# Kernel optimization log

Hardware: AMD Instinct MI355X
Metric: run time of the kernel (lower is better)

Reference implementation:

```python
import jax, jax.numpy as jnp
from jax import lax
import numpy as np

B0 = 2          # batch
S = 32          # spatial grid side; L = S*S + 2
L = S * S + 2
DM = 256        # d_model
ED = 512        # d_inner = expand_factor * d_model
N = 16          # d_state
R = 16          # dt_rank = ceil(d_model/16)
K = 4           # d_conv


def _dwconv(x, w, b):
    # x: (B, L, ED) -> causal depthwise conv1d, kernel K, left-pad K-1 (== torch pad K-1 then [:, :, :L])
    xt = jnp.transpose(x, (0, 2, 1))  # (B, ED, L)
    o = lax.conv_general_dilated(xt, w, (1,), [(K - 1, 0)],
                                 feature_group_count=ED,
                                 dimension_numbers=('NCH', 'OIH', 'NCH'))
    return jnp.transpose(o + b[None, :, None], (0, 2, 1))


def _ssm(x, Alog, Dp, xp_w, dt_w, dt_b):
    # x: (B, L, ED); selective scan (mamba.py math, pscan=True path)
    A = -jnp.exp(Alog)                       # (ED, N)
    dBC = x @ xp_w.T                          # (B, L, R+2N)
    delta = jax.nn.softplus(dBC[..., :R] @ dt_w.T + dt_b)  # (B, L, ED)
    Bm = dBC[..., R:R + N]                    # (B, L, N)
    Cm = dBC[..., R + N:]                     # (B, L, N)
    dA = jnp.exp(delta[..., None] * A)        # (B, L, ED, N)
    dBx = (delta * x)[..., None] * Bm[:, :, None, :]  # (B, L, ED, N)

    def comb(e1, e2):
        a1, b1 = e1
        a2, b2 = e2
        return a1 * a2, a2 * b1 + b2

    _, hs = lax.associative_scan(comb, (dA, dBx), axis=1)  # h_t = dA_t*h_{t-1} + dBx_t
    return jnp.einsum('blen,bln->ble', hs, Cm) + Dp * x


def _cross(t):
    # keep first/last token, transpose the SxS interior grid (row-major <-> col-major)
    b, l, d = t.shape
    inner = t[:, 1:-1].reshape(b, S, S, d).transpose(0, 2, 1, 3).reshape(b, S * S, d)
    return jnp.concatenate([t[:, :1], inner, t[:, -1:]], axis=1)


def _branch(xz, cw, cb, xp, dw, db, Al, Dp):
    xa, za = jnp.split(xz, 2, axis=-1)
    xa = jax.nn.silu(_dwconv(xa, cw, cb))
    return _ssm(xa, Al, Dp, xp, dw, db) * jax.nn.silu(za)


def _forward(x, in_w, out_w, *p):
    xz = x @ in_w.T  # (B, L, 2*ED)
    (cwa, cba, xpa, dwa, dba, Ala, Da,
     cwb, cbb, xpb, dwb, dbb, Alb, Db,
     cwc, cbc, xpc, dwc, dbc, Alc, Dc,
     cwd, cbd, xpd, dwd, dbd, Ald, Dd) = p
    ga = _branch(xz, cwa, cba, xpa, dwa, dba, Ala, Da)                # forward scan
    gb = _branch(xz[:, ::-1], cwb, cbb, xpb, dwb, dbb, Alb, Db)       # reversed scan
    xzc = _cross(xz)
    gc = _branch(xzc, cwc, cbc, xpc, dwc, dbc, Alc, Dc)               # transposed scan
    gd = _branch(xzc[:, ::-1], cwd, cbd, xpd, dwd, dbd, Ald, Dd)      # reversed-transposed scan
    # gating commutes with token permutations, so reassemble gated outputs
    y = (ga + gb[:, ::-1] + _cross(gc) + _cross(gd)[:, ::-1]) * 0.25  # divide_output=True
    return y @ out_w.T


def setup_inputs() -> dict:
    keys = jax.random.split(jax.random.key(0), 64)
    it = iter(keys)

    def nrm(shape, scale=0.02):
        return scale * jax.random.normal(next(it), shape, dtype=jnp.float32)

    d = {}
    d['x'] = jax.random.normal(next(it), (B0, L, DM), dtype=jnp.float32)
    d['in_w'] = nrm((2 * ED, DM))
    d['out_w'] = nrm((DM, ED))
    std = R ** -0.5
    for s in ['a', 'b', 'c', 'd']:
        d[f'conv_w_{s}'] = nrm((ED, 1, K), 0.1)
        d[f'conv_b_{s}'] = jnp.zeros((ED,), jnp.float32)
        d[f'xp_w_{s}'] = nrm((R + 2 * N, ED))
        d[f'dt_w_{s}'] = jax.random.uniform(next(it), (ED, R), minval=-std, maxval=std, dtype=jnp.float32)
        dt = jnp.exp(jax.random.uniform(next(it), (ED,), dtype=jnp.float32)
                     * (np.float32(np.log(0.1)) - np.float32(np.log(0.001))) + np.float32(np.log(0.001)))
        d[f'dt_b_{s}'] = dt + jnp.log(-jnp.expm1(-dt))  # inverse-softplus init
        d[f'Alog_{s}'] = jnp.log(jnp.tile(jnp.arange(1, N + 1, dtype=jnp.float32), (ED, 1)))
        d[f'D_{s}'] = jnp.ones((ED,), jnp.float32)
    return d


def reference(x, in_w, out_w,
              conv_w_a, conv_b_a, xp_w_a, dt_w_a, dt_b_a, Alog_a, D_a,
              conv_w_b, conv_b_b, xp_w_b, dt_w_b, dt_b_b, Alog_b, D_b,
              conv_w_c, conv_b_c, xp_w_c, dt_w_c, dt_b_c, Alog_c, D_c,
              conv_w_d, conv_b_d, xp_w_d, dt_w_d, dt_b_d, Alog_d, D_d):
    return _forward(x, in_w, out_w,
                    conv_w_a, conv_b_a, xp_w_a, dt_w_a, dt_b_a, Alog_a, D_a,
                    conv_w_b, conv_b_b, xp_w_b, dt_w_b, dt_b_b, Alog_b, D_b,
                    conv_w_c, conv_b_c, xp_w_c, dt_w_c, dt_b_c, Alog_c, D_c,
                    conv_w_d, conv_b_d, xp_w_d, dt_w_d, dt_b_d, Alog_d, D_d)
```

## Files before the change

### kernel.cpp

```cpp
#include <hip/hip_runtime.h>
#include <math.h>

#define LL 1026
#define EDim 512
#define MM 2052
#define NC 8
#define LC 128

struct Params {
  const float* cw[4];
  const float* cb[4];
  const float* xpw[4];
  const float* dtw[4];
  const float* dtb[4];
  const float* Al[4];
  const float* Dp[4];
};

__device__ __forceinline__ int sigma_map(int branch, int l) {
  if (branch & 1) l = LL - 1 - l;
  if (branch & 2) {
    if (l > 0 && l < LL - 1) {
      int p = l - 1;
      l = 1 + ((p & 31) << 5) + (p >> 5);
    }
  }
  return l;
}

__device__ __forceinline__ float silu_f(float v) { return v / (1.f + expf(-v)); }

template<int CTRL>
__device__ __forceinline__ float dpp_mov0(float x) {
  int r = __builtin_amdgcn_update_dpp(0, __float_as_int(x), CTRL, 0xF, 0xF, false);
  return __int_as_float(r);
}

__global__ __launch_bounds__(256) void k1_gemm_in(
    const float* __restrict__ x, const float* __restrict__ w,
    float* __restrict__ xa, float* __restrict__ sz) {
  __shared__ float As[32][65];
  __shared__ float Bs[32][65];
  const int t = threadIdx.x;
  const int tx = t & 15, ty = t >> 4;
  const int m0 = blockIdx.x * 64, n0 = blockIdx.y * 64;
  float acc[4][4] = {};
  for (int k0 = 0; k0 < 256; k0 += 32) {
    #pragma unroll
    for (int p = 0; p < 2; ++p) {
      int f = t + p * 256;
      int row = f >> 3, cf = f & 7;
      int gr = m0 + row; gr = gr < MM ? gr : MM - 1;
      float4 v = *(const float4*)(x + (size_t)gr * 256 + k0 + cf * 4);
      As[cf*4+0][row] = v.x; As[cf*4+1][row] = v.y;
      As[cf*4+2][row] = v.z; As[cf*4+3][row] = v.w;
      int gn = n0 + row;
      float4 u = *(const float4*)(w + (size_t)gn * 256 + k0 + cf * 4);
      Bs[cf*4+0][row] = u.x; Bs[cf*4+1][row] = u.y;
      Bs[cf*4+2][row] = u.z; Bs[cf*4+3][row] = u.w;
    }
    __syncthreads();
    #pragma unroll
    for (int k = 0; k < 32; ++k) {
      float a0 = As[k][ty*4+0], a1 = As[k][ty*4+1], a2 = As[k][ty*4+2], a3 = As[k][ty*4+3];
      float b0 = Bs[k][tx*4+0], b1 = Bs[k][tx*4+1], b2 = Bs[k][tx*4+2], b3 = Bs[k][tx*4+3];
      acc[0][0]=fmaf(a0,b0,acc[0][0]); acc[0][1]=fmaf(a0,b1,acc[0][1]); acc[0][2]=fmaf(a0,b2,acc[0][2]); acc[0][3]=fmaf(a0,b3,acc[0][3]);
      acc[1][0]=fmaf(a1,b0,acc[1][0]); acc[1][1]=fmaf(a1,b1,acc[1][1]); acc[1][2]=fmaf(a1,b2,acc[1][2]); acc[1][3]=fmaf(a1,b3,acc[1][3]);
      acc[2][0]=fmaf(a2,b0,acc[2][0]); acc[2][1]=fmaf(a2,b1,acc[2][1]); acc[2][2]=fmaf(a2,b2,acc[2][2]); acc[2][3]=fmaf(a2,b3,acc[2][3]);
      acc[3][0]=fmaf(a3,b0,acc[3][0]); acc[3][1]=fmaf(a3,b1,acc[3][1]); acc[3][2]=fmaf(a3,b2,acc[3][2]); acc[3][3]=fmaf(a3,b3,acc[3][3]);
    }
    __syncthreads();
  }
  #pragma unroll
  for (int i = 0; i < 4; ++i) {
    int gm = m0 + ty*4 + i;
    if (gm < MM) {
      #pragma unroll
      for (int j = 0; j < 4; ++j) {
        int gn = n0 + tx*4 + j;
        float v = acc[i][j];
        if (gn < 512) xa[(size_t)gm*512 + gn] = v;
        else          sz[(size_t)gm*512 + gn - 512] = silu_f(v);
      }
    }
  }
}

__global__ __launch_bounds__(256) void k2_branch(
    Params P, const float* __restrict__ xa,
    float* __restrict__ xac, float* __restrict__ delta, float* __restrict__ bcg) {
  __shared__ float xcS[16][516];
  __shared__ float dBCs[16][49];
  const int t = threadIdx.x;
  const int l0 = blockIdx.x * 16;
  const int b  = blockIdx.y;
  const int br = blockIdx.z;
  const int e0 = 2 * t;
  const float* cw = P.cw[br];
  const float w00 = cw[e0*4+0], w01 = cw[e0*4+1], w02 = cw[e0*4+2], w03 = cw[e0*4+3];
  const float w10 = cw[(e0+1)*4+0], w11 = cw[(e0+1)*4+1], w12 = cw[(e0+1)*4+2], w13 = cw[(e0+1)*4+3];
  const float cb0 = P.cb[br][e0], cb1 = P.cb[br][e0+1];
  const float* xab = xa + (size_t)b * LL * 512;
  const size_t obase = (size_t)(br*2 + b) * LL;

  float h0x=0,h0y=0,h1x=0,h1y=0,h2x=0,h2y=0,h3x=0,h3y=0;
  for (int i = -3; i < 16; ++i) {
    int l = l0 + i;
    float cx = 0.f, cy = 0.f;
    if (l >= 0 && l < LL) {
      int pos = sigma_map(br, l);
      float2 v = *(const float2*)(xab + (size_t)pos * 512 + e0);
      cx = v.x; cy = v.y;
    }
    h0x=h1x; h0y=h1y; h1x=h2x; h1y=h2y; h2x=h3x; h2y=h3y; h3x=cx; h3y=cy;
    if (i >= 0) {
      float o0 = fmaf(w00,h0x, fmaf(w01,h1x, fmaf(w02,h2x, fmaf(w03,h3x, cb0))));
      float o1 = fmaf(w10,h0y, fmaf(w11,h1y, fmaf(w12,h2y, fmaf(w13,h3y, cb1))));
      o0 = silu_f(o0); o1 = silu_f(o1);
      *(float2*)&xcS[i][e0] = make_float2(o0, o1);
      if (l < LL)
        *(float2*)(xac + (obase + l) * 512 + e0) = make_float2(o0, o1);
    }
  }
  __syncthreads();

  const int rowi = t & 15;
  const int r0 = t >> 4;
  const float* xpw = P.xpw[br];
  const float4* xr4 = (const float4*)&xcS[rowi][0];
  const float4* wa = (const float4*)(xpw + (size_t)r0 * 512);
  const float4* wb = (const float4*)(xpw + (size_t)(r0 + 16) * 512);
  const float4* wc = (const float4*)(xpw + (size_t)(r0 + 32) * 512);
  float acc0 = 0.f, acc1 = 0.f, acc2 = 0.f;
  #pragma unroll 8
  for (int e4 = 0; e4 < 128; ++e4) {
    float4 xv = xr4[e4];
    float4 a = wa[e4], bb = wb[e4], c = wc[e4];
    acc0 = fmaf(xv.x,a.x, fmaf(xv.y,a.y, fmaf(xv.z,a.z, fmaf(xv.w,a.w, acc0))));
    acc1 = fmaf(xv.x,bb.x,fmaf(xv.y,bb.y,fmaf(xv.z,bb.z,fmaf(xv.w,bb.w,acc1))));
    acc2 = fmaf(xv.x,c.x, fmaf(xv.y,c.y, fmaf(xv.z,c.z, fmaf(xv.w,c.w, acc2))));
  }
  dBCs[rowi][r0]      = acc0;
  dBCs[rowi][r0 + 16] = acc1;
  dBCs[rowi][r0 + 32] = acc2;
  __syncthreads();

  for (int idx = t; idx < 512; idx += 256) {
    int row = idx >> 5, c = idx & 31;
    int l = l0 + row;
    if (l < LL) bcg[(obase + l)*32 + c] = dBCs[row][16 + c];
  }

  const float* dtw = P.dtw[br];
  float dw0[16], dw1[16];
  #pragma unroll
  for (int r = 0; r < 16; ++r) { dw0[r] = dtw[e0*16 + r]; dw1[r] = dtw[(e0+1)*16 + r]; }
  const float db0 = P.dtb[br][e0], db1 = P.dtb[br][e0+1];
  for (int row = 0; row < 16; ++row) {
    int l = l0 + row;
    if (l >= LL) break;
    float s0 = db0, s1 = db1;
    #pragma unroll
    for (int r = 0; r < 16; ++r) {
      float d = dBCs[row][r];
      s0 = fmaf(d, dw0[r], s0);
      s1 = fmaf(d, dw1[r], s1);
    }
    float sp0 = fmaxf(s0, 0.f) + log1pf(expf(-fabsf(s0)));
    float sp1 = fmaxf(s1, 0.f) + log1pf(expf(-fabsf(s1)));
    *(float2*)(delta + (obase + l)*512 + e0) = make_float2(sp0, sp1);
  }
}

__global__ __launch_bounds__(256) void k3a_chunk(
    Params P, const float* __restrict__ xac, const float* __restrict__ delta,
    const float* __restrict__ bcg, float* __restrict__ Pc, float* __restrict__ Qc) {
  __shared__ float dT[16][33], xT[16][33], bT[16][33];
  const int t = threadIdx.x;
  const int eL = t >> 4, n = t & 15;
  const int e0 = blockIdx.x * 16;
  const int b = blockIdx.y;
  const int br = blockIdx.z / NC, c = blockIdx.z % NC;
  const size_t sbase = (size_t)(br*2 + b) * LL;
  const float* dl = delta + sbase * 512;
  const float* xc = xac + sbase * 512;
  const float* bc = bcg + sbase * 32;
  const float A_en = -expf(P.Al[br][(e0 + eL)*16 + n]);
  const int l0 = c * LC;
  const int lend = (c == NC-1) ? LL : (l0 + LC);
  float h = 0.f, dsum = 0.f;

  for (int c0 = l0; c0 < lend; c0 += 32) {
    #pragma unroll
    for (int p = 0; p < 2; ++p) {
      int idx = t + p*256;
      int s = idx >> 4, ee = idx & 15;
      int l = c0 + s;
      float dv = 0.f, xv = 0.f, bv = 0.f;
      if (l < lend) {
        dv = dl[(size_t)l*512 + e0 + ee];
        xv = xc[(size_t)l*512 + e0 + ee];
        bv = bc[l*32 + ee];
      }
      dT[ee][s] = dv; xT[ee][s] = xv; bT[ee][s] = bv;
    }
    __syncthreads();
    float da[32], dbx[32];
    #pragma unroll
    for (int s = 0; s < 32; ++s) {
      float d = dT[eL][s];
      da[s]  = __expf(d * A_en);
      dbx[s] = d * xT[eL][s] * bT[n][s];
      dsum += d;
    }
    #pragma unroll
    for (int s = 0; s < 32; ++s) h = fmaf(da[s], h, dbx[s]);
    __syncthreads();
  }
  size_t oi = ((((size_t)(br*2 + b)*NC + c)*32 + blockIdx.x)*256 + t);
  Pc[oi] = __expf(dsum * A_en);
  Qc[oi] = h;
}

__global__ __launch_bounds__(256) void k3b_scan(
    Params P, const float* __restrict__ xac, const float* __restrict__ delta,
    const float* __restrict__ bcg, const float* __restrict__ sz,
    const float* __restrict__ Pc, const float* __restrict__ Qc,
    float* __restrict__ g) {
  __shared__ float dT[16][33], xT[16][33], bT[16][33], cT[16][33];
  __shared__ float ybuf[32][17];
  const int t = threadIdx.x;
  const int eL = t >> 4, n = t & 15;
  const int e0 = blockIdx.x * 16;
  const int b = blockIdx.y;
  const int br = blockIdx.z / NC, c = blockIdx.z % NC;
  const size_t sbase = (size_t)(br*2 + b) * LL;
  const float* dl = delta + sbase * 512;
  const float* xc = xac + sbase * 512;
  const float* bc = bcg + sbase * 32;
  const float A_en = -expf(P.Al[br][(e0 + eL)*16 + n]);
  const float Dval = P.Dp[br][e0 + (t & 15)];
  const float* szb = sz + (size_t)b * LL * 512;
  float* gb = g + (size_t)br * MM * 512 + (size_t)b * LL * 512;

  float h = 0.f;
  for (int cc = 0; cc < c; ++cc) {
    size_t ii = ((((size_t)(br*2 + b)*NC + cc)*32 + blockIdx.x)*256 + t);
    h = fmaf(Pc[ii], h, Qc[ii]);
  }

  const int l0c = c * LC;
  const int lend = (c == NC-1) ? LL : (l0c + LC);
  for (int c0 = l0c; c0 < lend; c0 += 32) {
    #pragma unroll
    for (int p = 0; p < 2; ++p) {
      int idx = t + p*256;
      int s = idx >> 4, ee = idx & 15;
      int l = c0 + s;
      float dv = 0.f, xv = 0.f, bv = 0.f, cv = 0.f;
      if (l < lend) {
        dv = dl[(size_t)l*512 + e0 + ee];
        xv = xc[(size_t)l*512 + e0 + ee];
        bv = bc[l*32 + ee];
        cv = bc[l*32 + 16 + ee];
      }
      dT[ee][s] = dv; xT[ee][s] = xv; bT[ee][s] = bv; cT[ee][s] = cv;
    }
    __syncthreads();

    float da[32], dbx[32], ccv[32];
    #pragma unroll
    for (int s = 0; s < 32; ++s) {
      float d  = dT[eL][s];
      float xv = xT[eL][s];
      da[s]  = __expf(d * A_en);
      dbx[s] = d * xv * bT[n][s];
      ccv[s] = cT[n][s];
    }
    #pragma unroll
    for (int s = 0; s < 32; ++s) {
      h = fmaf(da[s], h, dbx[s]);
      float r = h * ccv[s];
      r += dpp_mov0<0xB1>(r);
      r += dpp_mov0<0x4E>(r);
      r += dpp_mov0<0x114>(r);
      r += dpp_mov0<0x118>(r);
      if (n == 15) ybuf[s][eL] = r;
    }
    __syncthreads();

    #pragma unroll
    for (int p = 0; p < 2; ++p) {
      int idx = t + p*256;
      int s = idx >> 4, ee = idx & 15;
      int l = c0 + s;
      if (l < lend) {
        float yv = fmaf(Dval, xT[ee][s], ybuf[s][ee]);
        int pos = sigma_map(br, l);
        float szv = szb[(size_t)pos * 512 + e0 + ee];
        gb[(size_t)pos * 512 + e0 + ee] = yv * szv;
      }
    }
    __syncthreads();
  }
}

__global__ __launch_bounds__(256) void k4_gemm_out(
    const float* __restrict__ g, const float* __restrict__ w, float* __restrict__ out) {
  __shared__ float As[32][65];
  __shared__ float Bs[32][33];
  const int t = threadIdx.x;
  const int tx = t & 15, ty = t >> 4;
  const int m0 = blockIdx.x * 64, n0 = blockIdx.y * 32;
  const float* g1 = g + (size_t)MM*512;
  const float* g2 = g + (size_t)2*MM*512;
  const float* g3 = g + (size_t)3*MM*512;
  float acc[4][2] = {};
  for (int k0 = 0; k0 < 512; k0 += 32) {
    #pragma unroll
    for (int p = 0; p < 8; ++p) {
      int idx = t + p*256;
      int row = idx >> 5, kk = idx & 31;
      int gm = m0 + row; gm = gm < MM ? gm : MM - 1;
      size_t ga = (size_t)gm*512 + k0 + kk;
      As[kk][row] = 0.25f * (g[ga] + g1[ga] + g2[ga] + g3[ga]);
    }
    #pragma unroll
    for (int p = 0; p < 4; ++p) {
      int idx = t + p*256;
      int row = idx >> 5, kk = idx & 31;
      Bs[kk][row] = w[(size_t)(n0 + row)*512 + k0 + kk];
    }
    __syncthreads();
    #pragma unroll
    for (int k = 0; k < 32; ++k) {
      float a0 = As[k][ty*4+0], a1 = As[k][ty*4+1], a2 = As[k][ty*4+2], a3 = As[k][ty*4+3];
      float b0 = Bs[k][tx*2+0], b1 = Bs[k][tx*2+1];
      acc[0][0]=fmaf(a0,b0,acc[0][0]); acc[0][1]=fmaf(a0,b1,acc[0][1]);
      acc[1][0]=fmaf(a1,b0,acc[1][0]); acc[1][1]=fmaf(a1,b1,acc[1][1]);
      acc[2][0]=fmaf(a2,b0,acc[2][0]); acc[2][1]=fmaf(a2,b1,acc[2][1]);
      acc[3][0]=fmaf(a3,b0,acc[3][0]); acc[3][1]=fmaf(a3,b1,acc[3][1]);
    }
    __syncthreads();
  }
  #pragma unroll
  for (int i = 0; i < 4; ++i) {
    int gm = m0 + ty*4 + i;
    if (gm < MM) {
      out[(size_t)gm*256 + n0 + tx*2 + 0] = acc[i][0];
      out[(size_t)gm*256 + n0 + tx*2 + 1] = acc[i][1];
    }
  }
}

extern "C" void kernel_launch(void* const* d_in, const int* in_sizes, int n_in,
                              void* d_out, int out_size, void* d_ws, size_t ws_size,
                              hipStream_t stream) {
  const float* x    = (const float*)d_in[0];
  const float* in_w = (const float*)d_in[1];
  const float* out_w= (const float*)d_in[2];
  Params prm;
  for (int s = 0; s < 4; ++s) {
    prm.cw[s]  = (const float*)d_in[3 + s*7 + 0];
    prm.cb[s]  = (const float*)d_in[3 + s*7 + 1];
    prm.xpw[s] = (const float*)d_in[3 + s*7 + 2];
    prm.dtw[s] = (const float*)d_in[3 + s*7 + 3];
    prm.dtb[s] = (const float*)d_in[3 + s*7 + 4];
    prm.Al[s]  = (const float*)d_in[3 + s*7 + 5];
    prm.Dp[s]  = (const float*)d_in[3 + s*7 + 6];
  }
  float* ws = (float*)d_ws;
  const size_t SZ1 = (size_t)MM * 512;
  float* xa   = ws;
  float* szp  = ws + SZ1;
  float* xac  = ws + 2*SZ1;
  float* dlt  = ws + 6*SZ1;
  float* bc   = ws + 10*SZ1;
  float* gbuf = ws + 10*SZ1 + (size_t)4*MM*32;
  float* Pc = xa;
  float* Qc = xa + (size_t)8*NC*32*256;

  k1_gemm_in<<<dim3(33, 16), 256, 0, stream>>>(x, in_w, xa, szp);
  k2_branch <<<dim3(65, 2, 4), 256, 0, stream>>>(prm, xa, xac, dlt, bc);
  k3a_chunk <<<dim3(32, 2, 4*NC), 256, 0, stream>>>(prm, xac, dlt, bc, Pc, Qc);
  k3b_scan  <<<dim3(32, 2, 4*NC), 256, 0, stream>>>(prm, xac, dlt, bc, szp, Pc, Qc, gbuf);
  k4_gemm_out<<<dim3(33, 8), 256, 0, stream>>>(gbuf, out_w, (float*)d_out);
}
```

Before: 330.5 us.

## Shrink k2 and k4 tiles for more blocks; vectorize shared loads in GEMMs

```diff
diff --git a/kernel.cpp b/kernel.cpp
--- a/kernel.cpp
+++ b/kernel.cpp
@@ -39,8 +39,8 @@
 __global__ __launch_bounds__(256) void k1_gemm_in(
     const float* __restrict__ x, const float* __restrict__ w,
     float* __restrict__ xa, float* __restrict__ sz) {
-  __shared__ float As[32][65];
-  __shared__ float Bs[32][65];
+  __shared__ float As[32][68];
+  __shared__ float Bs[32][68];
   const int t = threadIdx.x;
   const int tx = t & 15, ty = t >> 4;
   const int m0 = blockIdx.x * 64, n0 = blockIdx.y * 64;
@@ -62,8 +62,10 @@
     __syncthreads();
     #pragma unroll
     for (int k = 0; k < 32; ++k) {
-      float a0 = As[k][ty*4+0], a1 = As[k][ty*4+1], a2 = As[k][ty*4+2], a3 = As[k][ty*4+3];
-      float b0 = Bs[k][tx*4+0], b1 = Bs[k][tx*4+1], b2 = Bs[k][tx*4+2], b3 = Bs[k][tx*4+3];
+      float4 av = *(const float4*)&As[k][ty*4];
+      float4 bv = *(const float4*)&Bs[k][tx*4];
+      float a0 = av.x, a1 = av.y, a2 = av.z, a3 = av.w;
+      float b0 = bv.x, b1 = bv.y, b2 = bv.z, b3 = bv.w;
       acc[0][0]=fmaf(a0,b0,acc[0][0]); acc[0][1]=fmaf(a0,b1,acc[0][1]); acc[0][2]=fmaf(a0,b2,acc[0][2]); acc[0][3]=fmaf(a0,b3,acc[0][3]);
       acc[1][0]=fmaf(a1,b0,acc[1][0]); acc[1][1]=fmaf(a1,b1,acc[1][1]); acc[1][2]=fmaf(a1,b2,acc[1][2]); acc[1][3]=fmaf(a1,b3,acc[1][3]);
       acc[2][0]=fmaf(a2,b0,acc[2][0]); acc[2][1]=fmaf(a2,b1,acc[2][1]); acc[2][2]=fmaf(a2,b2,acc[2][2]); acc[2][3]=fmaf(a2,b3,acc[2][3]);
@@ -89,10 +91,10 @@
 __global__ __launch_bounds__(256) void k2_branch(
     Params P, const float* __restrict__ xa,
     float* __restrict__ xac, float* __restrict__ delta, float* __restrict__ bcg) {
-  __shared__ float xcS[16][516];
-  __shared__ float dBCs[16][49];
-  const int t = threadIdx.x;
-  const int l0 = blockIdx.x * 16;
+  __shared__ float xcS[8][516];
+  __shared__ float dBCs[8][2][52];
+  const int t = threadIdx.x;
+  const int l0 = blockIdx.x * 8;
   const int b  = blockIdx.y;
   const int br = blockIdx.z;
   const int e0 = 2 * t;
@@ -104,7 +106,7 @@
   const size_t obase = (size_t)(br*2 + b) * LL;
 
   float h0x=0,h0y=0,h1x=0,h1y=0,h2x=0,h2y=0,h3x=0,h3y=0;
-  for (int i = -3; i < 16; ++i) {
+  for (int i = -3; i < 8; ++i) {
     int l = l0 + i;
     float cx = 0.f, cy = 0.f;
     if (l >= 0 && l < LL) {
@@ -124,31 +126,33 @@
   }
   __syncthreads();
 
-  const int rowi = t & 15;
-  const int r0 = t >> 4;
+  const int combo = t & 15;
+  const int prow = combo >> 1, phalf = combo & 1;
+  const int tg = t >> 4;
   const float* xpw = P.xpw[br];
-  const float4* xr4 = (const float4*)&xcS[rowi][0];
-  const float4* wa = (const float4*)(xpw + (size_t)r0 * 512);
-  const float4* wb = (const float4*)(xpw + (size_t)(r0 + 16) * 512);
-  const float4* wc = (const float4*)(xpw + (size_t)(r0 + 32) * 512);
+  const float4* xr4 = (const float4*)&xcS[prow][phalf*256];
+  const float4* wa = (const float4*)(xpw + (size_t)tg*512        + phalf*256);
+  const float4* wb = (const float4*)(xpw + (size_t)(tg+16)*512   + phalf*256);
+  const float4* wc = (const float4*)(xpw + (size_t)(tg+32)*512   + phalf*256);
   float acc0 = 0.f, acc1 = 0.f, acc2 = 0.f;
   #pragma unroll 8
-  for (int e4 = 0; e4 < 128; ++e4) {
+  for (int e4 = 0; e4 < 64; ++e4) {
     float4 xv = xr4[e4];
     float4 a = wa[e4], bb = wb[e4], c = wc[e4];
     acc0 = fmaf(xv.x,a.x, fmaf(xv.y,a.y, fmaf(xv.z,a.z, fmaf(xv.w,a.w, acc0))));
     acc1 = fmaf(xv.x,bb.x,fmaf(xv.y,bb.y,fmaf(xv.z,bb.z,fmaf(xv.w,bb.w,acc1))));
     acc2 = fmaf(xv.x,c.x, fmaf(xv.y,c.y, fmaf(xv.z,c.z, fmaf(xv.w,c.w, acc2))));
   }
-  dBCs[rowi][r0]      = acc0;
-  dBCs[rowi][r0 + 16] = acc1;
-  dBCs[rowi][r0 + 32] = acc2;
+  dBCs[prow][phalf][tg]      = acc0;
+  dBCs[prow][phalf][tg + 16] = acc1;
+  dBCs[prow][phalf][tg + 32] = acc2;
   __syncthreads();
 
-  for (int idx = t; idx < 512; idx += 256) {
-    int row = idx >> 5, c = idx & 31;
+  {
+    int row = t >> 5, c = t & 31;
     int l = l0 + row;
-    if (l < LL) bcg[(obase + l)*32 + c] = dBCs[row][16 + c];
+    if (l < LL)
+      bcg[(obase + l)*32 + c] = dBCs[row][0][16 + c] + dBCs[row][1][16 + c];
   }
 
   const float* dtw = P.dtw[br];
@@ -156,13 +160,13 @@
   #pragma unroll
   for (int r = 0; r < 16; ++r) { dw0[r] = dtw[e0*16 + r]; dw1[r] = dtw[(e0+1)*16 + r]; }
   const float db0 = P.dtb[br][e0], db1 = P.dtb[br][e0+1];
-  for (int row = 0; row < 16; ++row) {
+  for (int row = 0; row < 8; ++row) {
     int l = l0 + row;
     if (l >= LL) break;
     float s0 = db0, s1 = db1;
     #pragma unroll
     for (int r = 0; r < 16; ++r) {
-      float d = dBCs[row][r];
+      float d = dBCs[row][0][r] + dBCs[row][1][r];
       s0 = fmaf(d, dw0[r], s0);
       s1 = fmaf(d, dw1[r], s1);
     }
@@ -307,18 +311,18 @@
 
 __global__ __launch_bounds__(256) void k4_gemm_out(
     const float* __restrict__ g, const float* __restrict__ w, float* __restrict__ out) {
-  __shared__ float As[32][65];
-  __shared__ float Bs[32][33];
+  __shared__ float As[32][38];
+  __shared__ float Bs[32][38];
   const int t = threadIdx.x;
   const int tx = t & 15, ty = t >> 4;
-  const int m0 = blockIdx.x * 64, n0 = blockIdx.y * 32;
+  const int m0 = blockIdx.x * 32, n0 = blockIdx.y * 32;
   const float* g1 = g + (size_t)MM*512;
   const float* g2 = g + (size_t)2*MM*512;
   const float* g3 = g + (size_t)3*MM*512;
-  float acc[4][2] = {};
+  float acc[2][2] = {};
   for (int k0 = 0; k0 < 512; k0 += 32) {
     #pragma unroll
-    for (int p = 0; p < 8; ++p) {
+    for (int p = 0; p < 4; ++p) {
       int idx = t + p*256;
       int row = idx >> 5, kk = idx & 31;
       int gm = m0 + row; gm = gm < MM ? gm : MM - 1;
@@ -334,21 +338,20 @@
     __syncthreads();
     #pragma unroll
     for (int k = 0; k < 32; ++k) {
-      float a0 = As[k][ty*4+0], a1 = As[k][ty*4+1], a2 = As[k][ty*4+2], a3 = As[k][ty*4+3];
-      float b0 = Bs[k][tx*2+0], b1 = Bs[k][tx*2+1];
-      acc[0][0]=fmaf(a0,b0,acc[0][0]); acc[0][1]=fmaf(a0,b1,acc[0][1]);
-      acc[1][0]=fmaf(a1,b0,acc[1][0]); acc[1][1]=fmaf(a1,b1,acc[1][1]);
-      acc[2][0]=fmaf(a2,b0,acc[2][0]); acc[2][1]=fmaf(a2,b1,acc[2][1]);
-      acc[3][0]=fmaf(a3,b0,acc[3][0]); acc[3][1]=fmaf(a3,b1,acc[3][1]);
+      float2 av = *(const float2*)&As[k][ty*2];
+      float2 bv = *(const float2*)&Bs[k][tx*2];
+      acc[0][0]=fmaf(av.x,bv.x,acc[0][0]); acc[0][1]=fmaf(av.x,bv.y,acc[0][1]);
+      acc[1][0]=fmaf(av.y,bv.x,acc[1][0]); acc[1][1]=fmaf(av.y,bv.y,acc[1][1]);
     }
     __syncthreads();
   }
   #pragma unroll
-  for (int i = 0; i < 4; ++i) {
-    int gm = m0 + ty*4 + i;
+  for (int i = 0; i < 2; ++i) {
+    int gm = m0 + ty*2 + i;
     if (gm < MM) {
-      out[(size_t)gm*256 + n0 + tx*2 + 0] = acc[i][0];
-      out[(size_t)gm*256 + n0 + tx*2 + 1] = acc[i][1];
+      #pragma unroll
+      for (int j = 0; j < 2; ++j)
+        out[(size_t)gm*256 + n0 + tx*2 + j] = acc[i][j];
     }
   }
 }
@@ -381,8 +384,8 @@
   float* Qc = xa + (size_t)8*NC*32*256;
 
   k1_gemm_in<<<dim3(33, 16), 256, 0, stream>>>(x, in_w, xa, szp);
-  k2_branch <<<dim3(65, 2, 4), 256, 0, stream>>>(prm, xa, xac, dlt, bc);
+  k2_branch <<<dim3(129, 2, 4), 256, 0, stream>>>(prm, xa, xac, dlt, bc);
   k3a_chunk <<<dim3(32, 2, 4*NC), 256, 0, stream>>>(prm, xac, dlt, bc, Pc, Qc);
   k3b_scan  <<<dim3(32, 2, 4*NC), 256, 0, stream>>>(prm, xac, dlt, bc, szp, Pc, Qc, gbuf);
-  k4_gemm_out<<<dim3(33, 8), 256, 0, stream>>>(gbuf, out_w, (float*)d_out);
-}
+  k4_gemm_out<<<dim3(65, 8), 256, 0, stream>>>(gbuf, out_w, (float*)d_out);
+}
```

Result: no change. 326.4 us (-1.2%).
